# Performance work log

Hardware: AMD Instinct MI355X
Metric: run time of the kernel (lower is better)

## Reference

```python
import jax, jax.numpy as jnp
import numpy as np

NEG = -10000.0
B, S, NL = 512, 1024, 49   # batch, seq_len, raw label count
L = NL + 2                  # label_size with <start>, <end>


def setup_inputs() -> dict:
    key = jax.random.key(0)
    k1, k2, k3, k4 = jax.random.split(key, 4)
    logits = jax.random.normal(k1, (B, S, NL), jnp.float32)
    transition = jax.random.normal(k2, (L, L), jnp.float32)
    # structural constraints from CRF.initialize(): nothing transitions into <end> row-wise,
    # nothing leaves <start> (transition[to, from] convention of the original code)
    transition = transition.at[:, L - 1].set(NEG).at[L - 2, :].set(NEG)
    labels = jax.random.randint(k3, (B, S), 0, NL, dtype=jnp.int32)
    lens = jax.random.randint(k4, (B,), 1, S + 1, dtype=jnp.int32)
    return {"logits": logits, "transition": transition, "labels": labels, "lens": lens}


def _seq_mask(lens, max_len):
    return jnp.arange(max_len)[None, :] < lens[:, None]


def _crf_loglik(logits, transition, labels, lens):
    b, s, nl = logits.shape
    l = transition.shape[0]
    start, end = l - 2, l - 1
    # pad_logits: append -10000 scores for <start>/<end>
    lg = jnp.concatenate([logits, jnp.full((b, s, 2), NEG, logits.dtype)], axis=2)  # [B,S,L]
    # ---- gold unary score ----
    unary = jnp.take_along_axis(lg, labels[:, :, None], axis=2)[..., 0]  # [B,S]
    unary = jnp.where(_seq_mask(lens, s), unary, 0.0).sum(axis=1)
    # ---- gold binary (transition) score ----
    ext = jnp.concatenate(
        [jnp.full((b, 1), start, labels.dtype), labels, jnp.full((b, 1), end, labels.dtype)], axis=1
    )  # [B,S+2]
    ext = jnp.where(_seq_mask(lens + 1, s + 2), ext, end)
    trn_scr = transition[ext[:, 1:], ext[:, :-1]]  # [B,S+1]; transition[to, from]
    binary = jnp.where(_seq_mask(lens + 1, s + 1), trn_scr, 0.0).sum(axis=1)
    gold = unary + binary
    # ---- partition function via forward-algorithm scan ----
    alpha0 = jnp.full((b, l), NEG, logits.dtype).at[:, start].set(0.0)
    def step(carry, logit_t):
        alpha, t = carry
        # mat[b,i,j] = logit_t[b,i] + alpha[b,j] + transition[i,j]
        mat = logit_t[:, :, None] + alpha[:, None, :] + transition[None, :, :]
        alpha_nxt = jax.scipy.special.logsumexp(mat, axis=2)
        alpha = jnp.where((t < lens)[:, None], alpha_nxt, alpha)
        return (alpha, t + 1), None
    (alpha, _), _ = jax.lax.scan(step, (alpha0, jnp.zeros((), lens.dtype)), jnp.swapaxes(lg, 0, 1))
    norm = jax.scipy.special.logsumexp(alpha + transition[end][None, :], axis=1)  # [B]
    return gold - norm


def reference(logits, transition, labels, lens):
    # CRF log-likelihood per sequence: gold path score minus log partition
    return _crf_loglik(logits, transition, labels, lens)
```

## Files before the change

kernel.cpp:

```cpp
#include <hip/hip_runtime.h>

#define NEGV (-10000.0f)

constexpr int B_ = 512;
constexpr int S_ = 1024;
constexpr int NL_ = 49;
constexpr int L_ = 51;

__device__ __forceinline__ float readlane_f(float v, int l) {
    return __int_as_float(__builtin_amdgcn_readlane(__float_as_int(v), l));
}

template <int CTRL>
__device__ __forceinline__ float dpp_max_step(float v) {
    int sh = __builtin_amdgcn_update_dpp(__float_as_int(v), __float_as_int(v),
                                         CTRL, 0xf, 0xf, false);
    return fmaxf(v, __int_as_float(sh));
}

__device__ __forceinline__ float wave_max_sgpr(float v) {
    v = dpp_max_step<0x111>(v);
    v = dpp_max_step<0x112>(v);
    v = dpp_max_step<0x114>(v);
    v = dpp_max_step<0x118>(v);
    v = dpp_max_step<0x142>(v);
    v = dpp_max_step<0x143>(v);
    return readlane_f(v, 63);
}

__global__ __launch_bounds__(64, 1) void crf_fwd(
    const float* __restrict__ logits,
    const float* __restrict__ transition,
    const int*   __restrict__ labels,
    const int*   __restrict__ lens,
    float*       __restrict__ out)
{
    const int b    = blockIdx.x;
    const int lane = threadIdx.x;
    const int len  = __builtin_amdgcn_readfirstlane(lens[b]);

    const float* __restrict__ lg  = logits + (size_t)b * (S_ * NL_);
    const int*   __restrict__ lab = labels + (size_t)b * S_;

    float Erow[NL_];
    float Tend, estart;
    {
        const bool st = (lane < NL_);
        const float* trow = transition + ((lane < L_) ? lane : 0) * L_;
        #pragma unroll
        for (int j = 0; j < NL_; ++j) {
            float tv = trow[j];
            Erow[j] = st ? __expf(tv) : 0.0f;
        }
        estart = __expf(trow[NL_]);
        Tend   = (lane < L_) ? transition[(L_ - 1) * L_ + lane] : NEGV;
    }

    float g = 0.0f;
    for (int t = lane; t < S_; t += 64) {
        if (t < len) {
            int c = lab[t];
            int p = (t == 0) ? (L_ - 2) : lab[t - 1];
            g += lg[t * NL_ + c] + transition[c * L_ + p];
            if (t == len - 1) g += transition[(L_ - 1) * L_ + c];
        }
    }
    #pragma unroll
    for (int o = 32; o >= 1; o >>= 1) g += __shfl_xor(g, o, 64);

    float alpha;
    {
        float lg0 = (lane < NL_) ? lg[lane] : NEGV;
        alpha = (lane < NL_) ? (lg0 + __logf(estart)) : NEGV;
    }
    float M = 0.0f;

    auto loadlg = [&](int t) -> float {
        float v = NEGV;
        if (lane < NL_) v = lg[t * NL_ + lane];
        return v;
    };

    float buf0 = loadlg(1);
    float buf1 = loadlg(2);
    float buf2 = loadlg(3);
    float buf3 = loadlg(4);

    auto substep = [&](float cur, int t) {
        float p  = __expf(alpha - M);
        float Mn = wave_max_sgpr(alpha);
        float y0 = 0.f, y1 = 0.f, y2 = 0.f, y3 = 0.f;
        #pragma unroll
        for (int j = 0; j < 48; j += 4) {
            y0 = fmaf(readlane_f(p, j + 0), Erow[j + 0], y0);
            y1 = fmaf(readlane_f(p, j + 1), Erow[j + 1], y1);
            y2 = fmaf(readlane_f(p, j + 2), Erow[j + 2], y2);
            y3 = fmaf(readlane_f(p, j + 3), Erow[j + 3], y3);
        }
        y0 = fmaf(readlane_f(p, 48), Erow[48], y0);
        float y = (y0 + y1) + (y2 + y3);
        float anew = cur + M + __logf(y);
        if (t < len && lane < NL_) alpha = anew;
        M = Mn;
    };

    const int tEnd = 1 + (((len - 1) + 3) & ~3);
    for (int t = 1; t < tEnd; t += 4) {
        int t4 = t + 4; t4 = (t4 < S_) ? t4 : (S_ - 1);
        int t5 = t + 5; t5 = (t5 < S_) ? t5 : (S_ - 1);
        int t6 = t + 6; t6 = (t6 < S_) ? t6 : (S_ - 1);
        int t7 = t + 7; t7 = (t7 < S_) ? t7 : (S_ - 1);
        substep(buf0, t + 0); buf0 = loadlg(t4);
        substep(buf1, t + 1); buf1 = loadlg(t5);
        substep(buf2, t + 2); buf2 = loadlg(t6);
        substep(buf3, t + 3); buf3 = loadlg(t7);
    }

    float x = (lane < L_) ? (alpha + Tend) : NEGV;
    float mx = x;
    #pragma unroll
    for (int o = 32; o >= 1; o >>= 1) mx = fmaxf(mx, __shfl_xor(mx, o, 64));
    float e = __expf(x - mx);
    #pragma unroll
    for (int o = 32; o >= 1; o >>= 1) e += __shfl_xor(e, o, 64);
    float norm = mx + __logf(e);

    if (lane == 0) out[b] = g - norm;
}

extern "C" void kernel_launch(void* const* d_in, const int* in_sizes, int n_in,
                              void* d_out, int out_size, void* d_ws, size_t ws_size,
                              hipStream_t stream) {
    const float* logits     = (const float*)d_in[0];
    const float* transition = (const float*)d_in[1];
    const int*   labels     = (const int*)d_in[2];
    const int*   lens       = (const int*)d_in[3];
    float*       out        = (float*)d_out;
    crf_fwd<<<dim3(B_), dim3(64), 0, stream>>>(logits, transition, labels, lens, out);
}
```

Measured before the change: 522.1 us.

## Broadcast alpha probabilities via LDS float4 reads instead of readlane

Each step now writes the exponentiated alpha vector into a double-buffered shared array and reads it back as 13 float4 broadcast loads, replacing 49 scalar readlane operations. The logit prefetch depth also grows from 4 to 8 steps. The aim is to cut the serial readlane and SGPR-to-VALU dependency chain on each recurrence step. In exchange it adds an LDS store-to-load round trip, whose latency sits on the critical path, and relies on single-wave execution for ordering since there are no barriers.

```diff
diff --git a/kernel.cpp b/kernel.cpp
--- a/kernel.cpp
+++ b/kernel.cpp
@@ -42,6 +42,8 @@
     const float* __restrict__ lg  = logits + (size_t)b * (S_ * NL_);
     const int*   __restrict__ lab = labels + (size_t)b * S_;
 
+    __shared__ __align__(16) float pbuf[2][52];
+
     float Erow[NL_];
     float Tend, estart;
     {
@@ -81,39 +83,50 @@
         return v;
     };
 
-    float buf0 = loadlg(1);
-    float buf1 = loadlg(2);
-    float buf2 = loadlg(3);
-    float buf3 = loadlg(4);
+    float b0 = loadlg(1), b1 = loadlg(2), b2 = loadlg(3), b3 = loadlg(4);
+    float b4 = loadlg(5), b5 = loadlg(6), b6 = loadlg(7), b7 = loadlg(8);
 
-    auto substep = [&](float cur, int t) {
-        float p  = __expf(alpha - M);
+    auto substep = [&](float cur, int t, int par) {
+        float p = __expf(alpha - M);
+        if (lane < NL_) pbuf[par][lane] = p;
         float Mn = wave_max_sgpr(alpha);
+        const float4* pv = (const float4*)pbuf[par];
+        float4 q[13];
+        #pragma unroll
+        for (int k = 0; k < 13; ++k) q[k] = pv[k];
         float y0 = 0.f, y1 = 0.f, y2 = 0.f, y3 = 0.f;
         #pragma unroll
-        for (int j = 0; j < 48; j += 4) {
-            y0 = fmaf(readlane_f(p, j + 0), Erow[j + 0], y0);
-            y1 = fmaf(readlane_f(p, j + 1), Erow[j + 1], y1);
-            y2 = fmaf(readlane_f(p, j + 2), Erow[j + 2], y2);
-            y3 = fmaf(readlane_f(p, j + 3), Erow[j + 3], y3);
+        for (int k = 0; k < 12; ++k) {
+            y0 = fmaf(q[k].x, Erow[4 * k + 0], y0);
+            y1 = fmaf(q[k].y, Erow[4 * k + 1], y1);
+            y2 = fmaf(q[k].z, Erow[4 * k + 2], y2);
+            y3 = fmaf(q[k].w, Erow[4 * k + 3], y3);
         }
-        y0 = fmaf(readlane_f(p, 48), Erow[48], y0);
+        y0 = fmaf(q[12].x, Erow[48], y0);
         float y = (y0 + y1) + (y2 + y3);
         float anew = cur + M + __logf(y);
         if (t < len && lane < NL_) alpha = anew;
         M = Mn;
     };
 
-    const int tEnd = 1 + (((len - 1) + 3) & ~3);
-    for (int t = 1; t < tEnd; t += 4) {
-        int t4 = t + 4; t4 = (t4 < S_) ? t4 : (S_ - 1);
-        int t5 = t + 5; t5 = (t5 < S_) ? t5 : (S_ - 1);
-        int t6 = t + 6; t6 = (t6 < S_) ? t6 : (S_ - 1);
-        int t7 = t + 7; t7 = (t7 < S_) ? t7 : (S_ - 1);
-        substep(buf0, t + 0); buf0 = loadlg(t4);
-        substep(buf1, t + 1); buf1 = loadlg(t5);
-        substep(buf2, t + 2); buf2 = loadlg(t6);
-        substep(buf3, t + 3); buf3 = loadlg(t7);
+    const int tEnd = 1 + (((len - 1) + 7) & ~7);
+    for (int t = 1; t < tEnd; t += 8) {
+        int t8  = t + 8;  t8  = (t8  < S_) ? t8  : (S_ - 1);
+        int t9  = t + 9;  t9  = (t9  < S_) ? t9  : (S_ - 1);
+        int t10 = t + 10; t10 = (t10 < S_) ? t10 : (S_ - 1);
+        int t11 = t + 11; t11 = (t11 < S_) ? t11 : (S_ - 1);
+        int t12 = t + 12; t12 = (t12 < S_) ? t12 : (S_ - 1);
+        int t13 = t + 13; t13 = (t13 < S_) ? t13 : (S_ - 1);
+        int t14 = t + 14; t14 = (t14 < S_) ? t14 : (S_ - 1);
+        int t15 = t + 15; t15 = (t15 < S_) ? t15 : (S_ - 1);
+        substep(b0, t + 0, 0); b0 = loadlg(t8);
+        substep(b1, t + 1, 1); b1 = loadlg(t9);
+        substep(b2, t + 2, 0); b2 = loadlg(t10);
+        substep(b3, t + 3, 1); b3 = loadlg(t11);
+        substep(b4, t + 4, 0); b4 = loadlg(t12);
+        substep(b5, t + 5, 1); b5 = loadlg(t13);
+        substep(b6, t + 6, 0); b6 = loadlg(t14);
+        substep(b7, t + 7, 1); b7 = loadlg(t15);
     }
 
     float x = (lane < L_) ? (alpha + Tend) : NEGV;
```

Result: slower. 632.1 us (+21.1%).
